# Kernel optimization log

Measured on AMD Instinct MI355X. Metric: run time of the kernel, lower is better.

The kernel has to match this reference:

```python
import jax, jax.numpy as jnp
import numpy as np

N = 32768          # nodes
DEG = 16           # fixed in-degree per dst node
E = N * DEG        # edges
IN_FEATS = 256
HEADS = 4
OUT = 64
NUM_CLASSES = 40
SLOPE = 0.2        # leaky_relu negative slope
GM = 0.1           # graph margin
CM = 0.1           # class margin


def setup_inputs() -> dict:
    key = jax.random.key(0)
    ks = jax.random.split(key, 8)
    feat = jax.random.normal(ks[0], (N, IN_FEATS), dtype=jnp.float32)
    label = jax.random.randint(ks[1], (N,), 0, NUM_CLASSES)
    src = jax.random.randint(ks[2], (E,), 0, N)
    # dst sorted with fixed in-degree DEG -> dense mailboxes of shape [N, DEG, ...]
    dst = jnp.repeat(jnp.arange(N), DEG)
    # negative graph: same src, dst permuted (construct_negative_graph, k=1)
    neg_perm = jax.random.permutation(ks[3], E)
    scale_w = (2.0 / (IN_FEATS + HEADS * OUT)) ** 0.5  # xavier-ish
    W = jax.random.normal(ks[4], (HEADS * OUT, IN_FEATS), dtype=jnp.float32) * scale_w
    scale_a = (2.0 / (1 + OUT)) ** 0.5
    attn_l = jax.random.normal(ks[5], (HEADS, OUT), dtype=jnp.float32) * scale_a
    attn_r = jax.random.normal(ks[6], (HEADS, OUT), dtype=jnp.float32) * scale_a
    return {"feat": feat, "label": label, "src": src, "dst": dst,
            "neg_perm": neg_perm, "W": W, "attn_l": attn_l, "attn_r": attn_r}


def _leaky(x):
    return jnp.where(x >= 0, x, SLOPE * x)


def reference(feat, label, src, dst, neg_perm, W, attn_l, attn_r):
    n = feat.shape[0]
    e_count = src.shape[0]
    deg = e_count // n
    H, D = attn_l.shape

    feat_src = (feat @ W.T).reshape(n, H, D)               # [N,H,D]
    el = jnp.einsum('nhd,hd->nh', feat_src, attn_l)        # [N,H]
    er = jnp.einsum('nhd,hd->nh', feat_src, attn_r)        # [N,H]
    e = _leaky(el[src] + er[dst])                          # [E,H]

    # ---- graph loss (negative sampling margin) ----
    neg_dst = dst[neg_perm]
    ne = _leaky(el[src] + er[neg_dst])                     # [E,H]
    pw = e.reshape(n, deg, H)                              # positive msgs per dst
    nw = ne.reshape(n, deg, H)                             # negative msgs per dst
    Lg = jnp.maximum(nw[:, :, None, :] + GM - pw[:, None, :, :], 0.0).sum() / (n * H)

    # ---- boundary (class) loss: same-label vs diff-label neighbors ----
    adj = (label[src] == label[dst]).reshape(n, deg)       # [N,DEG] bool
    # difference[n,a,b,h] = w[n,b,h] + CM - w[n,a,h], valid iff adj[a] & ~adj[b]
    val = jnp.maximum(pw[:, None, :, :] + CM - pw[:, :, None, :], 0.0)
    mask = (adj[:, :, None] & (~adj[:, None, :]))[..., None]
    Lb = jnp.where(mask, val, 0.0).sum() / (n * H)

    # ---- edge softmax over each dst's in-edges + attention-weighted sum ----
    a = jax.nn.softmax(pw, axis=1)                         # [N,DEG,H]
    ft = feat_src[src].reshape(n, deg, H, D)               # gathered src feats
    rst = jnp.einsum('ndh,ndhf->nhf', a, ft)               # [N,H,D]
    return rst, Lg, Lb
```

## Files before the change

### kernel.cpp

```cpp
#include <hip/hip_runtime.h>
#include <hip/hip_bf16.h>

#define N_NODES 32768
#define DEG 16
#define E_EDGES (N_NODES * DEG)
#define HEADS 4
#define OUT_D 64
#define HD 256
#define SLOPE 0.2f
#define GMARG 0.1f
#define CMARG 0.1f
#define LOSS_BLOCKS 2048

typedef float f32x4 __attribute__((ext_vector_type(4)));
typedef unsigned short ushort4v __attribute__((ext_vector_type(4)));
typedef unsigned short ushort8v __attribute__((ext_vector_type(8)));
typedef short bf16x8 __attribute__((ext_vector_type(8)));
typedef short short4v __attribute__((ext_vector_type(4)));

__device__ __forceinline__ float bf2f(unsigned short u) {
    return __uint_as_float(((unsigned int)u) << 16);
}
__device__ __forceinline__ unsigned short f2bf(float x) {
    __hip_bfloat16 h = __float2bfloat16(x);
    return __builtin_bit_cast(unsigned short, h);
}
__device__ __forceinline__ short f2bf_s(float x) {
    __hip_bfloat16 h = __float2bfloat16(x);
    return __builtin_bit_cast(short, h);
}
__device__ __forceinline__ float leaky(float x) {
    return x >= 0.f ? x : SLOPE * x;
}
__device__ __forceinline__ void gl_lds16(const void* g, void* l) {
    __builtin_amdgcn_global_load_lds(
        (__attribute__((address_space(1))) void*)(g),
        (__attribute__((address_space(3))) void*)(l), 16, 0, 0);
}

__global__ void badcfg_kernel(float* out, float code) {
    out[0] = code;
}

__global__ __launch_bounds__(256) void convw_kernel(const float* __restrict__ W,
                                                    short* __restrict__ Wb) {
    const int i = (blockIdx.x * 256 + threadIdx.x) * 4;
    f32x4 v = *(const f32x4*)(W + i);
    short4v o;
    o[0] = f2bf_s(v[0]); o[1] = f2bf_s(v[1]); o[2] = f2bf_s(v[2]); o[3] = f2bf_s(v[3]);
    *(short4v*)(Wb + i) = o;
}

__global__ __launch_bounds__(256) void gemm_kernel(const float* __restrict__ feat,
                                                   const short* __restrict__ Wb,
                                                   const float* __restrict__ attn_l,
                                                   const float* __restrict__ attn_r,
                                                   unsigned short* __restrict__ fsb,
                                                   float* __restrict__ el,
                                                   float* __restrict__ er) {
    __shared__ short s_b[2][16384];

    const int tid = threadIdx.x;
    const int wave = tid >> 6;
    const int lane = tid & 63;
    const int row0 = (blockIdx.x * 4 + wave) * 16;
    const int m = lane & 15;
    const int q = lane >> 4;

#pragma unroll
    for (int i = 0; i < 8; ++i) {
        const int sb = wave * 8 + i;
        const int kk2 = sb >> 4, t = sb & 15;
        const short* g = Wb + (size_t)(t * 16 + m) * HD + kk2 * 32 + q * 8;
        gl_lds16(g, &s_b[0][sb * 512]);
    }

    bf16x8 afr[8];
    const float* arow = feat + (size_t)(row0 + m) * HD + q * 8;
#pragma unroll
    for (int kk = 0; kk < 8; ++kk) {
        f32x4 lo = *(const f32x4*)(arow + kk * 32);
        f32x4 hi = *(const f32x4*)(arow + kk * 32 + 4);
        bf16x8 aa;
        aa[0] = f2bf_s(lo[0]); aa[1] = f2bf_s(lo[1]); aa[2] = f2bf_s(lo[2]); aa[3] = f2bf_s(lo[3]);
        aa[4] = f2bf_s(hi[0]); aa[5] = f2bf_s(hi[1]); aa[6] = f2bf_s(hi[2]); aa[7] = f2bf_s(hi[3]);
        afr[kk] = aa;
    }

    f32x4 acc[16];
#pragma unroll
    for (int t = 0; t < 16; ++t) acc[t] = (f32x4)(0.0f);

    __syncthreads();

#pragma unroll
    for (int c = 0; c < 4; ++c) {
        if (c < 3) {
#pragma unroll
            for (int i = 0; i < 8; ++i) {
                const int sb = wave * 8 + i;
                const int kk2 = sb >> 4, t = sb & 15;
                const short* g = Wb + (size_t)(t * 16 + m) * HD + (c + 1) * 64 + kk2 * 32 + q * 8;
                gl_lds16(g, &s_b[(c + 1) & 1][sb * 512]);
            }
        }
        const short* sbc = s_b[c & 1];
#pragma unroll
        for (int kk2 = 0; kk2 < 2; ++kk2) {
            const bf16x8 af = afr[c * 2 + kk2];
#pragma unroll
            for (int t = 0; t < 16; ++t) {
                bf16x8 bfr = *(const bf16x8*)(sbc + ((kk2 * 16 + t) * 64 + lane) * 8);
                acc[t] = __builtin_amdgcn_mfma_f32_16x16x32_bf16(af, bfr, acc[t], 0, 0, 0);
            }
        }
        __syncthreads();
    }

#pragma unroll
    for (int t = 0; t < 16; ++t) {
#pragma unroll
        for (int r = 0; r < 4; ++r) {
            fsb[(size_t)(row0 + q * 4 + r) * HD + t * 16 + m] = f2bf(acc[t][r]);
        }
    }

    float pel[4][4], per_[4][4];
#pragma unroll
    for (int h = 0; h < 4; ++h)
#pragma unroll
        for (int r = 0; r < 4; ++r) { pel[h][r] = 0.f; per_[h][r] = 0.f; }
#pragma unroll
    for (int t = 0; t < 16; ++t) {
        const float al = attn_l[t * 16 + m];
        const float ar = attn_r[t * 16 + m];
        const int h = t >> 2;
#pragma unroll
        for (int r = 0; r < 4; ++r) {
            pel[h][r] += acc[t][r] * al;
            per_[h][r] += acc[t][r] * ar;
        }
    }
#pragma unroll
    for (int mask = 1; mask < 16; mask <<= 1) {
#pragma unroll
        for (int h = 0; h < 4; ++h)
#pragma unroll
            for (int r = 0; r < 4; ++r) {
                pel[h][r] += __shfl_xor(pel[h][r], mask, 64);
                per_[h][r] += __shfl_xor(per_[h][r], mask, 64);
            }
    }
    if (m == 0) {
#pragma unroll
        for (int r = 0; r < 4; ++r) {
            const int node = row0 + q * 4 + r;
            f32x4 vl, vr;
            vl[0] = pel[0][r]; vl[1] = pel[1][r]; vl[2] = pel[2][r]; vl[3] = pel[3][r];
            vr[0] = per_[0][r]; vr[1] = per_[1][r]; vr[2] = per_[2][r]; vr[3] = per_[3][r];
            *(f32x4*)(el + (size_t)node * 4) = vl;
            *(f32x4*)(er + (size_t)node * 4) = vr;
        }
    }
}

__global__ __launch_bounds__(256) void fla_kernel(const int* __restrict__ src,
                                                  const int* __restrict__ perm,
                                                  const int* __restrict__ label,
                                                  const float* __restrict__ el,
                                                  const float* __restrict__ er,
                                                  const unsigned short* __restrict__ fsb,
                                                  float* __restrict__ out,
                                                  float* __restrict__ partials) {
    __shared__ float s_pw[16][17][4];
    __shared__ float s_a[16][17][4];
    __shared__ int   s_adj[16][17];
    __shared__ int   s_srcn[16][17];
    __shared__ float slg[4], slb[4];

    const int tid = threadIdx.x;
    const int wave = tid >> 6;
    const int lane = tid & 63;
    const int w = lane >> 4;
    const int a = lane & 15;
    const int nl = wave * 4 + w;
    const int n = blockIdx.x * 16 + nl;
    const int e = n * DEG + a;

    const int s  = src[e];
    const int nd = perm[e] >> 4;
    f32x4 els  = *(const f32x4*)(el + (size_t)s * 4);
    f32x4 ern  = *(const f32x4*)(er + (size_t)n * 4);
    f32x4 ernd = *(const f32x4*)(er + (size_t)nd * 4);
    const int adja = (label[s] == label[n]) ? 1 : 0;

    f32x4 pw, nw;
#pragma unroll
    for (int h = 0; h < 4; ++h) {
        pw[h] = leaky(els[h] + ern[h]);
        nw[h] = leaky(els[h] + ernd[h]);
    }
    *(f32x4*)&s_pw[nl][a][0] = pw;
    s_adj[nl][a] = adja;
    s_srcn[nl][a] = s;

    f32x4 mx = pw;
#pragma unroll
    for (int mask = 1; mask < 16; mask <<= 1)
#pragma unroll
        for (int h = 0; h < 4; ++h)
            mx[h] = fmaxf(mx[h], __shfl_xor(mx[h], mask, 64));
    f32x4 ee, sm;
#pragma unroll
    for (int h = 0; h < 4; ++h) { ee[h] = __expf(pw[h] - mx[h]); sm[h] = ee[h]; }
#pragma unroll
    for (int mask = 1; mask < 16; mask <<= 1)
#pragma unroll
        for (int h = 0; h < 4; ++h)
            sm[h] += __shfl_xor(sm[h], mask, 64);
    f32x4 aw;
#pragma unroll
    for (int h = 0; h < 4; ++h) aw[h] = ee[h] / sm[h];
    *(f32x4*)&s_a[nl][a][0] = aw;
    __syncthreads();

    float lg = 0.f, lb = 0.f;
#pragma unroll
    for (int b = 0; b < 16; ++b) {
        f32x4 pwb = *(const f32x4*)&s_pw[nl][b][0];
        const int adjb = s_adj[nl][b];
#pragma unroll
        for (int h = 0; h < 4; ++h)
            lg += fmaxf(nw[h] + GMARG - pwb[h], 0.f);
        if (adja && !adjb) {
#pragma unroll
            for (int h = 0; h < 4; ++h)
                lb += fmaxf(pwb[h] + CMARG - pw[h], 0.f);
        }
    }
#pragma unroll
    for (int mask = 1; mask < 64; mask <<= 1) {
        lg += __shfl_xor(lg, mask, 64);
        lb += __shfl_xor(lb, mask, 64);
    }
    if (lane == 0) { slg[wave] = lg; slb[wave] = lb; }
    __syncthreads();
    if (tid == 0) {
        partials[blockIdx.x * 2]     = slg[0] + slg[1] + slg[2] + slg[3];
        partials[blockIdx.x * 2 + 1] = slb[0] + slb[1] + slb[2] + slb[3];
    }

    const int nl2 = tid >> 4;
    const int tt  = tid & 15;
    const int hh  = tt >> 2;
    const int n2  = blockIdx.x * 16 + nl2;
    float acc[16];
#pragma unroll
    for (int k = 0; k < 16; ++k) acc[k] = 0.f;
#pragma unroll 4
    for (int j = 0; j < 16; ++j) {
        const int s2 = s_srcn[nl2][j];
        const float awj = s_a[nl2][j][hh];
        const unsigned short* rp = fsb + (size_t)s2 * HD + tt * 16;
        ushort8v u0 = *(const ushort8v*)(rp);
        ushort8v u1 = *(const ushort8v*)(rp + 8);
#pragma unroll
        for (int k = 0; k < 8; ++k) acc[k]     += awj * bf2f(u0[k]);
#pragma unroll
        for (int k = 0; k < 8; ++k) acc[8 + k] += awj * bf2f(u1[k]);
    }
    float* op = out + (size_t)n2 * HD + tt * 16;
#pragma unroll
    for (int i = 0; i < 4; ++i) {
        f32x4 v;
        v[0] = acc[i * 4]; v[1] = acc[i * 4 + 1]; v[2] = acc[i * 4 + 2]; v[3] = acc[i * 4 + 3];
        *(f32x4*)(op + i * 4) = v;
    }
}

__global__ __launch_bounds__(256) void finalize_kernel(const float* __restrict__ partials,
                                                       float* __restrict__ out) {
    const int tid = threadIdx.x;
    const int lane = tid & 63;
    const int wave = tid >> 6;
    double lg = 0.0, lb = 0.0;
    for (int i = tid; i < LOSS_BLOCKS; i += 256) {
        lg += (double)partials[i * 2];
        lb += (double)partials[i * 2 + 1];
    }
#pragma unroll
    for (int mask = 1; mask < 64; mask <<= 1) {
        lg += __shfl_xor(lg, mask, 64);
        lb += __shfl_xor(lb, mask, 64);
    }
    __shared__ double slg[4], slb[4];
    if (lane == 0) { slg[wave] = lg; slb[wave] = lb; }
    __syncthreads();
    if (tid == 0) {
        const double scale = 1.0 / (double)((size_t)N_NODES * HEADS);
        out[(size_t)N_NODES * HD]     = (float)((slg[0] + slg[1] + slg[2] + slg[3]) * scale);
        out[(size_t)N_NODES * HD + 1] = (float)((slb[0] + slb[1] + slb[2] + slb[3]) * scale);
    }
}

extern "C" void kernel_launch(void* const* d_in, const int* in_sizes, int n_in,
                              void* d_out, int out_size, void* d_ws, size_t ws_size,
                              hipStream_t stream) {
    const float* feat   = (const float*)d_in[0];
    const int*   label  = (const int*)d_in[1];
    const int*   src    = (const int*)d_in[2];
    const int*   perm   = (const int*)d_in[4];
    const float* W      = (const float*)d_in[5];
    const float* attn_l = (const float*)d_in[6];
    const float* attn_r = (const float*)d_in[7];
    float* out = (float*)d_out;

    const int expect[8] = {8388608, 32768, 524288, 524288, 524288, 65536, 256, 256};
    if (n_in != 8) {
        hipLaunchKernelGGL(badcfg_kernel, dim3(1), dim3(1), 0, stream, out, 60000.f);
        return;
    }
    for (int i = 0; i < 8; ++i) {
        if (in_sizes[i] != expect[i]) {
            hipLaunchKernelGGL(badcfg_kernel, dim3(1), dim3(1), 0, stream, out,
                               65536.f + 256.f * (float)i);
            return;
        }
    }
    if (out_size != N_NODES * HD + 2) {
        hipLaunchKernelGGL(badcfg_kernel, dim3(1), dim3(1), 0, stream, out, 200000.f);
        return;
    }

    char* ws = (char*)d_ws;
    size_t off = 0;
    float* partials = (float*)(ws + off); off += (size_t)LOSS_BLOCKS * 2 * sizeof(float);
    off = (off + 255) & ~(size_t)255;
    short* Wb = (short*)(ws + off); off += (size_t)HD * HD * sizeof(short);
    off = (off + 255) & ~(size_t)255;
    unsigned short* fsb = (unsigned short*)(ws + off); off += (size_t)N_NODES * HD * sizeof(unsigned short);
    float* el = (float*)(ws + off); off += (size_t)N_NODES * HEADS * sizeof(float);
    float* er = (float*)(ws + off); off += (size_t)N_NODES * HEADS * sizeof(float);
    if (off > ws_size) {
        hipLaunchKernelGGL(badcfg_kernel, dim3(1), dim3(1), 0, stream, out, 131072.f);
        return;
    }

    hipLaunchKernelGGL(convw_kernel, dim3(HD * HD / 1024), dim3(256), 0, stream, W, Wb);
    hipLaunchKernelGGL(gemm_kernel, dim3(N_NODES / 64), dim3(256), 0, stream,
                       feat, Wb, attn_l, attn_r, fsb, el, er);
    hipLaunchKernelGGL(fla_kernel, dim3(LOSS_BLOCKS), dim3(256), 0, stream,
                       src, perm, label, el, er, fsb, out, partials);
    hipLaunchKernelGGL(finalize_kernel, dim3(1), dim3(256), 0, stream, partials, out);
}
```

Baseline: 156.8 us.

## Load W fragments directly into registers and batch gather loads in aggregation

The GEMM kernel no longer stages W through LDS with global_load_lds and barriers. Each wave instead double-buffers B fragments in registers straight from global/L2, swaps the MFMA operand order so the output is transposed, writes bf16 rows with vector stores and computes el/er with fewer shuffles. The aggregation loop in fla_kernel issues 8 gather loads at a time before accumulating, to raise memory-level parallelism. The costs are higher register pressure, launch bounds that ask for 2 blocks, and each wave re-reading W from cache instead of sharing it through LDS.

```diff
diff --git a/kernel.cpp b/kernel.cpp
--- a/kernel.cpp
+++ b/kernel.cpp
@@ -32,11 +32,6 @@
 __device__ __forceinline__ float leaky(float x) {
     return x >= 0.f ? x : SLOPE * x;
 }
-__device__ __forceinline__ void gl_lds16(const void* g, void* l) {
-    __builtin_amdgcn_global_load_lds(
-        (__attribute__((address_space(1))) void*)(g),
-        (__attribute__((address_space(3))) void*)(l), 16, 0, 0);
-}
 
 __global__ void badcfg_kernel(float* out, float code) {
     out[0] = code;
@@ -51,29 +46,19 @@
     *(short4v*)(Wb + i) = o;
 }
 
-__global__ __launch_bounds__(256) void gemm_kernel(const float* __restrict__ feat,
-                                                   const short* __restrict__ Wb,
-                                                   const float* __restrict__ attn_l,
-                                                   const float* __restrict__ attn_r,
-                                                   unsigned short* __restrict__ fsb,
-                                                   float* __restrict__ el,
-                                                   float* __restrict__ er) {
-    __shared__ short s_b[2][16384];
-
+__global__ __launch_bounds__(256, 2) void gemm_kernel(const float* __restrict__ feat,
+                                                      const short* __restrict__ Wb,
+                                                      const float* __restrict__ attn_l,
+                                                      const float* __restrict__ attn_r,
+                                                      unsigned short* __restrict__ fsb,
+                                                      float* __restrict__ el,
+                                                      float* __restrict__ er) {
     const int tid = threadIdx.x;
     const int wave = tid >> 6;
     const int lane = tid & 63;
     const int row0 = (blockIdx.x * 4 + wave) * 16;
     const int m = lane & 15;
     const int q = lane >> 4;
-
-#pragma unroll
-    for (int i = 0; i < 8; ++i) {
-        const int sb = wave * 8 + i;
-        const int kk2 = sb >> 4, t = sb & 15;
-        const short* g = Wb + (size_t)(t * 16 + m) * HD + kk2 * 32 + q * 8;
-        gl_lds16(g, &s_b[0][sb * 512]);
-    }
 
     bf16x8 afr[8];
     const float* arow = feat + (size_t)(row0 + m) * HD + q * 8;
@@ -91,76 +76,68 @@
 #pragma unroll
     for (int t = 0; t < 16; ++t) acc[t] = (f32x4)(0.0f);
 
-    __syncthreads();
-
-#pragma unroll
-    for (int c = 0; c < 4; ++c) {
-        if (c < 3) {
-#pragma unroll
-            for (int i = 0; i < 8; ++i) {
-                const int sb = wave * 8 + i;
-                const int kk2 = sb >> 4, t = sb & 15;
-                const short* g = Wb + (size_t)(t * 16 + m) * HD + (c + 1) * 64 + kk2 * 32 + q * 8;
-                gl_lds16(g, &s_b[(c + 1) & 1][sb * 512]);
-            }
-        }
-        const short* sbc = s_b[c & 1];
-#pragma unroll
-        for (int kk2 = 0; kk2 < 2; ++kk2) {
-            const bf16x8 af = afr[c * 2 + kk2];
-#pragma unroll
-            for (int t = 0; t < 16; ++t) {
-                bf16x8 bfr = *(const bf16x8*)(sbc + ((kk2 * 16 + t) * 64 + lane) * 8);
-                acc[t] = __builtin_amdgcn_mfma_f32_16x16x32_bf16(af, bfr, acc[t], 0, 0, 0);
-            }
-        }
-        __syncthreads();
-    }
-
+    const short* wbase = Wb + (size_t)m * HD + q * 8;
+
+    bf16x8 p0[8], p1[8];
+#pragma unroll
+    for (int j = 0; j < 8; ++j)
+        p0[j] = *(const bf16x8*)(wbase + (size_t)j * 16 * HD);
+
+#pragma unroll
+    for (int g = 0; g < 16; ++g) {
+        const bf16x8* cur = ((g & 1) == 0) ? p0 : p1;
+        bf16x8* nxt       = ((g & 1) == 0) ? p1 : p0;
+        if (g < 15) {
+            const int gn = g + 1;
+            const int cn = gn >> 1;
+            const int tn0 = (gn & 1) * 8;
+#pragma unroll
+            for (int j = 0; j < 8; ++j)
+                nxt[j] = *(const bf16x8*)(wbase + (size_t)(tn0 + j) * 16 * HD + cn * 32);
+        }
+        const bf16x8 af = afr[g >> 1];
+        const int t0 = (g & 1) * 8;
+#pragma unroll
+        for (int j = 0; j < 8; ++j)
+            acc[t0 + j] = __builtin_amdgcn_mfma_f32_16x16x32_bf16(cur[j], af, acc[t0 + j], 0, 0, 0);
+    }
+
+    short* fsbs = (short*)fsb + (size_t)(row0 + m) * HD + q * 4;
 #pragma unroll
     for (int t = 0; t < 16; ++t) {
+        short4v o;
+        o[0] = f2bf_s(acc[t][0]); o[1] = f2bf_s(acc[t][1]);
+        o[2] = f2bf_s(acc[t][2]); o[3] = f2bf_s(acc[t][3]);
+        *(short4v*)(fsbs + t * 16) = o;
+    }
+
+    float pel[4], per_[4];
+#pragma unroll
+    for (int h = 0; h < 4; ++h) { pel[h] = 0.f; per_[h] = 0.f; }
+#pragma unroll
+    for (int t = 0; t < 16; ++t) {
+        f32x4 al4 = *(const f32x4*)(attn_l + t * 16 + q * 4);
+        f32x4 ar4 = *(const f32x4*)(attn_r + t * 16 + q * 4);
+        const int h = t >> 2;
 #pragma unroll
         for (int r = 0; r < 4; ++r) {
-            fsb[(size_t)(row0 + q * 4 + r) * HD + t * 16 + m] = f2bf(acc[t][r]);
-        }
-    }
-
-    float pel[4][4], per_[4][4];
-#pragma unroll
-    for (int h = 0; h < 4; ++h)
-#pragma unroll
-        for (int r = 0; r < 4; ++r) { pel[h][r] = 0.f; per_[h][r] = 0.f; }
-#pragma unroll
-    for (int t = 0; t < 16; ++t) {
-        const float al = attn_l[t * 16 + m];
-        const float ar = attn_r[t * 16 + m];
-        const int h = t >> 2;
-#pragma unroll
-        for (int r = 0; r < 4; ++r) {
-            pel[h][r] += acc[t][r] * al;
-            per_[h][r] += acc[t][r] * ar;
-        }
-    }
-#pragma unroll
-    for (int mask = 1; mask < 16; mask <<= 1) {
-#pragma unroll
-        for (int h = 0; h < 4; ++h)
-#pragma unroll
-            for (int r = 0; r < 4; ++r) {
-                pel[h][r] += __shfl_xor(pel[h][r], mask, 64);
-                per_[h][r] += __shfl_xor(per_[h][r], mask, 64);
-            }
-    }
-    if (m == 0) {
-#pragma unroll
-        for (int r = 0; r < 4; ++r) {
-            const int node = row0 + q * 4 + r;
-            f32x4 vl, vr;
-            vl[0] = pel[0][r]; vl[1] = pel[1][r]; vl[2] = pel[2][r]; vl[3] = pel[3][r];
-            vr[0] = per_[0][r]; vr[1] = per_[1][r]; vr[2] = per_[2][r]; vr[3] = per_[3][r];
-            *(f32x4*)(el + (size_t)node * 4) = vl;
-            *(f32x4*)(er + (size_t)node * 4) = vr;
-        }
+            pel[h] += acc[t][r] * al4[r];
+            per_[h] += acc[t][r] * ar4[r];
+        }
+    }
+#pragma unroll
+    for (int h = 0; h < 4; ++h) {
+        pel[h] += __shfl_xor(pel[h], 16, 64);
+        pel[h] += __shfl_xor(pel[h], 32, 64);
+        per_[h] += __shfl_xor(per_[h], 16, 64);
+        per_[h] += __shfl_xor(per_[h], 32, 64);
+    }
+    if (q == 0) {
+        f32x4 vl, vr;
+        vl[0] = pel[0]; vl[1] = pel[1]; vl[2] = pel[2]; vl[3] = pel[3];
+        vr[0] = per_[0]; vr[1] = per_[1]; vr[2] = per_[2]; vr[3] = per_[3];
+        *(f32x4*)(el + (size_t)(row0 + m) * 4) = vl;
+        *(f32x4*)(er + (size_t)(row0 + m) * 4) = vr;
     }
 }
 
@@ -257,17 +234,28 @@
     float acc[16];
 #pragma unroll
     for (int k = 0; k < 16; ++k) acc[k] = 0.f;
-#pragma unroll 4
-    for (int j = 0; j < 16; ++j) {
-        const int s2 = s_srcn[nl2][j];
-        const float awj = s_a[nl2][j][hh];
-        const unsigned short* rp = fsb + (size_t)s2 * HD + tt * 16;
-        ushort8v u0 = *(const ushort8v*)(rp);
-        ushort8v u1 = *(const ushort8v*)(rp + 8);
-#pragma unroll
-        for (int k = 0; k < 8; ++k) acc[k]     += awj * bf2f(u0[k]);
-#pragma unroll
-        for (int k = 0; k < 8; ++k) acc[8 + k] += awj * bf2f(u1[k]);
+
+#pragma unroll
+    for (int jo = 0; jo < 2; ++jo) {
+        ushort8v u0[8], u1[8];
+        float awj[8];
+#pragma unroll
+        for (int j2 = 0; j2 < 8; ++j2) {
+            const int j = jo * 8 + j2;
+            const int s2 = s_srcn[nl2][j];
+            awj[j2] = s_a[nl2][j][hh];
+            const unsigned short* rp = fsb + (size_t)s2 * HD + tt * 16;
+            u0[j2] = *(const ushort8v*)(rp);
+            u1[j2] = *(const ushort8v*)(rp + 8);
+        }
+#pragma unroll
+        for (int j2 = 0; j2 < 8; ++j2) {
+            const float awv = awj[j2];
+#pragma unroll
+            for (int k = 0; k < 8; ++k) acc[k]     += awv * bf2f(u0[j2][k]);
+#pragma unroll
+            for (int k = 0; k < 8; ++k) acc[8 + k] += awv * bf2f(u1[j2][k]);
+        }
     }
     float* op = out + (size_t)n2 * HD + tt * 16;
 #pragma unroll
```

After: 185.6 us. +18.4%, slower.

## Split fused loss/aggregation kernel and tile aggregation by head-channel group

Applied to the files above, without the earlier changes.

Splits the fused kernel into a loss kernel and a separate aggregation kernel. The aggregation kernel gives each block 128 nodes and one 32-channel slice of a single head, recomputing the softmax weights per head. The aim is to make neighbor feature gathers from a block touch a narrower column band, improving cache locality, and to raise parallelism. In exchange it adds a kernel launch, reloads src/el/er, and recomputes the attention logits.

```diff
diff --git a/kernel.cpp b/kernel.cpp
--- a/kernel.cpp
+++ b/kernel.cpp
@@ -13,6 +13,7 @@
 #define LOSS_BLOCKS 2048
 
 typedef float f32x4 __attribute__((ext_vector_type(4)));
+typedef int   int4v __attribute__((ext_vector_type(4)));
 typedef unsigned short ushort4v __attribute__((ext_vector_type(4)));
 typedef unsigned short ushort8v __attribute__((ext_vector_type(8)));
 typedef short bf16x8 __attribute__((ext_vector_type(8)));
@@ -164,18 +165,14 @@
     }
 }
 
-__global__ __launch_bounds__(256) void fla_kernel(const int* __restrict__ src,
-                                                  const int* __restrict__ perm,
-                                                  const int* __restrict__ label,
-                                                  const float* __restrict__ el,
-                                                  const float* __restrict__ er,
-                                                  const unsigned short* __restrict__ fsb,
-                                                  float* __restrict__ out,
-                                                  float* __restrict__ partials) {
-    __shared__ float s_pw[16][17][4];
-    __shared__ float s_a[16][17][4];
-    __shared__ int   s_adj[16][17];
-    __shared__ int   s_srcn[16][17];
+__global__ __launch_bounds__(256) void loss_kernel(const int* __restrict__ src,
+                                                   const int* __restrict__ perm,
+                                                   const int* __restrict__ label,
+                                                   const float* __restrict__ el,
+                                                   const float* __restrict__ er,
+                                                   float* __restrict__ partials) {
+    __shared__ float s_pw[16][16][4];
+    __shared__ int   s_adj[16][16];
     __shared__ float slg[4], slb[4];
 
     const int tid = threadIdx.x;
@@ -202,26 +199,6 @@
     }
     *(f32x4*)&s_pw[nl][a][0] = pw;
     s_adj[nl][a] = adja;
-    s_srcn[nl][a] = s;
-
-    f32x4 mx = pw;
-#pragma unroll
-    for (int mask = 1; mask < 16; mask <<= 1)
-#pragma unroll
-        for (int h = 0; h < 4; ++h)
-            mx[h] = fmaxf(mx[h], __shfl_xor(mx[h], mask, 64));
-    f32x4 ee, sm;
-#pragma unroll
-    for (int h = 0; h < 4; ++h) { ee[h] = __expf(pw[h] - mx[h]); sm[h] = ee[h]; }
-#pragma unroll
-    for (int mask = 1; mask < 16; mask <<= 1)
-#pragma unroll
-        for (int h = 0; h < 4; ++h)
-            sm[h] += __shfl_xor(sm[h], mask, 64);
-    f32x4 aw;
-#pragma unroll
-    for (int h = 0; h < 4; ++h) aw[h] = ee[h] / sm[h];
-    *(f32x4*)&s_a[nl][a][0] = aw;
     __syncthreads();
 
     float lg = 0.f, lb = 0.f;
@@ -249,19 +226,65 @@
         partials[blockIdx.x * 2]     = slg[0] + slg[1] + slg[2] + slg[3];
         partials[blockIdx.x * 2 + 1] = slb[0] + slb[1] + slb[2] + slb[3];
     }
-
-    const int nl2 = tid >> 4;
-    const int tt  = tid & 15;
-    const int hh  = tt >> 2;
-    const int n2  = blockIdx.x * 16 + nl2;
+}
+
+__global__ __launch_bounds__(256) void agg_kernel(const int* __restrict__ src,
+                                                  const float* __restrict__ el,
+                                                  const float* __restrict__ er,
+                                                  const unsigned short* __restrict__ fsb,
+                                                  float* __restrict__ out) {
+    __shared__ float s_a[16][128];
+    __shared__ int   s_s[16][128];
+
+    const int tid = threadIdx.x;
+    const int cg = blockIdx.x & 7;
+    const int ng = blockIdx.x >> 3;
+    const int hh = cg >> 1;
+
+    {
+        const int nl = tid >> 1;
+        const int j0 = (tid & 1) * 8;
+        const int n = ng * 128 + nl;
+        const int* sp = src + n * DEG + j0;
+        int4v sa = *(const int4v*)(sp);
+        int4v sb = *(const int4v*)(sp + 4);
+        int s8[8];
+        s8[0] = sa[0]; s8[1] = sa[1]; s8[2] = sa[2]; s8[3] = sa[3];
+        s8[4] = sb[0]; s8[5] = sb[1]; s8[6] = sb[2]; s8[7] = sb[3];
+        const float ernh = er[n * 4 + hh];
+        float pw[8];
+#pragma unroll
+        for (int k = 0; k < 8; ++k)
+            pw[k] = leaky(el[s8[k] * 4 + hh] + ernh);
+        float mx = pw[0];
+#pragma unroll
+        for (int k = 1; k < 8; ++k) mx = fmaxf(mx, pw[k]);
+        mx = fmaxf(mx, __shfl_xor(mx, 1, 64));
+        float ee[8], sum = 0.f;
+#pragma unroll
+        for (int k = 0; k < 8; ++k) { ee[k] = __expf(pw[k] - mx); sum += ee[k]; }
+        sum += __shfl_xor(sum, 1, 64);
+#pragma unroll
+        for (int k = 0; k < 8; ++k) {
+            s_a[j0 + k][nl] = ee[k] / sum;
+            s_s[j0 + k][nl] = s8[k];
+        }
+    }
+    __syncthreads();
+
+    const int nl2 = tid >> 1;
+    const int half = tid & 1;
+    const int n2 = ng * 128 + nl2;
+    const int chb = cg * 32 + half * 16;
+
     float acc[16];
 #pragma unroll
     for (int k = 0; k < 16; ++k) acc[k] = 0.f;
 #pragma unroll 4
     for (int j = 0; j < 16; ++j) {
-        const int s2 = s_srcn[nl2][j];
-        const float awj = s_a[nl2][j][hh];
-        const unsigned short* rp = fsb + (size_t)s2 * HD + tt * 16;
+        const int s2 = s_s[j][nl2];
+        const float awj = s_a[j][nl2];
+        const unsigned short* rp = fsb + (size_t)s2 * HD + chb;
         ushort8v u0 = *(const ushort8v*)(rp);
         ushort8v u1 = *(const ushort8v*)(rp + 8);
 #pragma unroll
@@ -269,7 +292,7 @@
 #pragma unroll
         for (int k = 0; k < 8; ++k) acc[8 + k] += awj * bf2f(u1[k]);
     }
-    float* op = out + (size_t)n2 * HD + tt * 16;
+    float* op = out + (size_t)n2 * HD + chb;
 #pragma unroll
     for (int i = 0; i < 4; ++i) {
         f32x4 v;
@@ -349,7 +372,9 @@
     hipLaunchKernelGGL(convw_kernel, dim3(HD * HD / 1024), dim3(256), 0, stream, W, Wb);
     hipLaunchKernelGGL(gemm_kernel, dim3(N_NODES / 64), dim3(256), 0, stream,
                        feat, Wb, attn_l, attn_r, fsb, el, er);
-    hipLaunchKernelGGL(fla_kernel, dim3(LOSS_BLOCKS), dim3(256), 0, stream,
-                       src, perm, label, el, er, fsb, out, partials);
+    hipLaunchKernelGGL(loss_kernel, dim3(LOSS_BLOCKS), dim3(256), 0, stream,
+                       src, perm, label, el, er, partials);
+    hipLaunchKernelGGL(agg_kernel, dim3(2048), dim3(256), 0, stream,
+                       src, el, er, fsb, out);
     hipLaunchKernelGGL(finalize_kernel, dim3(1), dim3(256), 0, stream, partials, out);
 }
```

Result: slower. 180.0 us (+14.8%).
